# Kernel optimization log

Measured on AMD Instinct MI355X. Metric: run time of the kernel, lower is better.

The kernel has to match this reference:

```python
import jax, jax.numpy as jnp
import numpy as np

ALPHA = 0.0  # module init alpha
BETA = 1.0   # default beta in set_target_with_data


def setup_inputs() -> dict:
    key = jax.random.key(0)
    k1, k2, k3, k4 = jax.random.split(key, 4)
    B, H, KP, N, D = 4, 16, 512, 4096, 64
    return {
        "K": jax.random.normal(k1, (B, H, KP, D), dtype=jnp.float32),
        "V": jax.random.normal(k2, (B, H, KP, D), dtype=jnp.float32),
        "xk": jax.random.normal(k3, (B, H, N, D), dtype=jnp.float32),
        "xv": jax.random.normal(k4, (B, H, N, D), dtype=jnp.float32),
    }


def reference(K, V, xk, xv):
    # set_target_with_data with dist_metric='dot', beta=1.0, beta2=None
    # dists: (B, H, k, n) = K @ xk^T
    dists = jnp.einsum('bhkd,bhnd->bhkn', K, xk)
    # softmax over the memory-slot axis (dim=-2)
    dk = jax.nn.softmax(BETA * dists, axis=-2)
    # normalize over the data axis (dim=-1)
    dkx = dk / jnp.sum(dk, axis=-1, keepdims=True)
    # weighted readout of data queries/values
    K_target = jnp.einsum('bhkn,bhnd->bhkd', dkx, xk)
    V_target = jnp.einsum('bhkn,bhnd->bhkd', dkx, xv)
    # set_target: grads used by maximize-SGD update
    gK = (1.0 - ALPHA) * (K_target - K)
    gV = (1.0 - ALPHA) * (V_target - V)
    return jnp.stack((gK, gV), axis=0)  # (2, B, H, k, d)
```

## Files before the change

### kernel.cpp

```cpp
#include <hip/hip_runtime.h>
#include <hip/hip_bf16.h>

typedef __bf16 bf16_t;
typedef __attribute__((ext_vector_type(8))) __bf16 bf16x8;
typedef __attribute__((ext_vector_type(4))) float f32x4;
typedef __attribute__((ext_vector_type(16))) float f32x16;

#define BH 64
#define KP 512
#define NN 4096
#define DD 64
#define GSZ (BH * KP * DD)
#define NT 64

#define MFMA16(a, b, c) __builtin_amdgcn_mfma_f32_16x16x32_bf16((a), (b), (c), 0, 0, 0)
#define MFMA32(a, b, c) __builtin_amdgcn_mfma_f32_32x32x16_bf16((a), (b), (c), 0, 0, 0)

__device__ __forceinline__ bf16x8 cvt8v(const f32x4 lo, const f32x4 hi) {
  bf16x8 r;
  r[0] = (bf16_t)lo[0]; r[1] = (bf16_t)lo[1]; r[2] = (bf16_t)lo[2]; r[3] = (bf16_t)lo[3];
  r[4] = (bf16_t)hi[0]; r[5] = (bf16_t)hi[1]; r[6] = (bf16_t)hi[2]; r[7] = (bf16_t)hi[3];
  return r;
}
__device__ __forceinline__ bf16x8 cvt8(const float* __restrict__ p) {
  return cvt8v(*(const f32x4*)p, *(const f32x4*)(p + 4));
}
__device__ __forceinline__ unsigned pack2(float a, float b) {
  union { bf16_t h[2]; unsigned u; } x;
  x.h[0] = (bf16_t)a; x.h[1] = (bf16_t)b;
  return x.u;
}

__device__ __forceinline__ void stage16(bf16_t* lds_base, const bf16_t* gsrc) {
  __builtin_amdgcn_global_load_lds(
      (const __attribute__((address_space(1))) void*)gsrc,
      (__attribute__((address_space(3))) void*)lds_base, 16, 0, 0);
}

__global__ __launch_bounds__(256) void hop_p1f(
    const float* __restrict__ Km, const float* __restrict__ xk,
    const float* __restrict__ xv,
    bf16_t* __restrict__ xk16, bf16_t* __restrict__ xkT16,
    bf16_t* __restrict__ xvT16, float* __restrict__ inv_colsum)
{
  __shared__ __align__(16) bf16_t Ks[128 * 72];
  bf16_t* T = Ks;

  const int tid  = threadIdx.x;
  const int wave = tid >> 6, lane = tid & 63;
  const int col  = lane & 15, quad = lane >> 4;
  const int bid  = blockIdx.x;
  const int bh   = (bid & 7) + 8 * ((bid >> 3) & 7);
  const int nblk = (bid >> 6) * 256;

  const float* Kb  = Km + (size_t)bh * KP * DD;
  const size_t gb  = (size_t)bh * NN * DD;
  const size_t gbT = (size_t)bh * DD * NN;

  const int row  = tid >> 2;
  const int d0   = (tid & 3) * 16;
  const int dcol = tid >> 2;
  const int nb   = (tid & 3) * 16;

  bf16x8 bf[4][2];

  #pragma unroll
  for (int b = 0; b < 4; b++) {
    const int nbase = nblk + b * 64;
    {
      const float* src = xk + gb + (size_t)(nbase + row) * DD + d0;
      const f32x4 a0 = *(const f32x4*)(src);
      const f32x4 a1 = *(const f32x4*)(src + 4);
      const f32x4 a2 = *(const f32x4*)(src + 8);
      const f32x4 a3 = *(const f32x4*)(src + 12);
      const bf16x8 lo = cvt8v(a0, a1), hi = cvt8v(a2, a3);
      bf16_t* dn = xk16 + gb + (size_t)(nbase + row) * DD + d0;
      *(bf16x8*)(dn)     = lo;
      *(bf16x8*)(dn + 8) = hi;
      *(bf16x8*)(T + row * 72 + d0)     = lo;
      *(bf16x8*)(T + row * 72 + d0 + 8) = hi;
    }
    __syncthreads();
    {
      bf16x8 o0, o1;
      #pragma unroll
      for (int j = 0; j < 8; j++) o0[j] = T[(nb + j) * 72 + dcol];
      #pragma unroll
      for (int j = 0; j < 8; j++) o1[j] = T[(nb + 8 + j) * 72 + dcol];
      bf16_t* dT = xkT16 + gbT + (size_t)dcol * NN + nbase + nb;
      *(bf16x8*)(dT)     = o0;
      *(bf16x8*)(dT + 8) = o1;
      if (wave == b) {
        #pragma unroll
        for (int nsub = 0; nsub < 4; nsub++) {
          bf[nsub][0] = *(const bf16x8*)(T + (nsub * 16 + col) * 72 + quad * 8);
          bf[nsub][1] = *(const bf16x8*)(T + (nsub * 16 + col) * 72 + 32 + quad * 8);
        }
      }
    }
    __syncthreads();
    {
      const float* src = xv + gb + (size_t)(nbase + row) * DD + d0;
      const f32x4 a0 = *(const f32x4*)(src);
      const f32x4 a1 = *(const f32x4*)(src + 4);
      const f32x4 a2 = *(const f32x4*)(src + 8);
      const f32x4 a3 = *(const f32x4*)(src + 12);
      *(bf16x8*)(T + row * 72 + d0)     = cvt8v(a0, a1);
      *(bf16x8*)(T + row * 72 + d0 + 8) = cvt8v(a2, a3);
    }
    __syncthreads();
    {
      bf16x8 o0, o1;
      #pragma unroll
      for (int j = 0; j < 8; j++) o0[j] = T[(nb + j) * 72 + dcol];
      #pragma unroll
      for (int j = 0; j < 8; j++) o1[j] = T[(nb + 8 + j) * 72 + dcol];
      bf16_t* dT = xvT16 + gbT + (size_t)dcol * NN + nbase + nb;
      *(bf16x8*)(dT)     = o0;
      *(bf16x8*)(dT + 8) = o1;
    }
    __syncthreads();
  }

  float colacc[4] = {0.f, 0.f, 0.f, 0.f};
  const int srow = tid >> 1, sdo = (tid & 1) * 32;

  for (int kc = 0; kc < KP; kc += 128) {
    __syncthreads();
    const float* src = Kb + (size_t)(kc + srow) * DD + sdo;
    #pragma unroll
    for (int u = 0; u < 4; u++) {
      const f32x4 p0 = *(const f32x4*)(src + 8 * u);
      const f32x4 p1 = *(const f32x4*)(src + 8 * u + 4);
      *(bf16x8*)(Ks + srow * 72 + sdo + 8 * u) = cvt8v(p0, p1);
    }
    __syncthreads();
    #pragma unroll
    for (int ks = 0; ks < 8; ks++) {
      const bf16x8 a0 = *(const bf16x8*)(Ks + (ks * 16 + col) * 72 + quad * 8);
      const bf16x8 a1 = *(const bf16x8*)(Ks + (ks * 16 + col) * 72 + 32 + quad * 8);
      #pragma unroll
      for (int nsub = 0; nsub < 4; nsub++) {
        f32x4 c = {0.f, 0.f, 0.f, 0.f};
        c = MFMA16(a0, bf[nsub][0], c);
        c = MFMA16(a1, bf[nsub][1], c);
        colacc[nsub] += __expf(c[0]) + __expf(c[1]) + __expf(c[2]) + __expf(c[3]);
      }
    }
  }
  #pragma unroll
  for (int nsub = 0; nsub < 4; nsub++) {
    colacc[nsub] += __shfl_xor(colacc[nsub], 16, 64);
    colacc[nsub] += __shfl_xor(colacc[nsub], 32, 64);
  }
  float v = colacc[0];
  v = (quad == 1) ? colacc[1] : v;
  v = (quad == 2) ? colacc[2] : v;
  v = (quad == 3) ? colacc[3] : v;
  inv_colsum[bh * NN + nblk + wave * 64 + quad * 16 + col] = 1.0f / v;
}

template <int NS>
__global__ __launch_bounds__(256) void hop_pass2s(
    const float* __restrict__ Km,
    const bf16_t* __restrict__ xk16, const bf16_t* __restrict__ xkT16,
    const bf16_t* __restrict__ xvT16,
    const float* __restrict__ inv_colsum,
    float* __restrict__ pK, float* __restrict__ pV, float* __restrict__ prs)
{
  constexpr int NSEG = NN / NS;

  __shared__ __align__(16) bf16_t xks[2][NT * DD];
  __shared__ __align__(16) bf16_t xkT[2][DD * NT];
  __shared__ __align__(16) bf16_t xvT[2][DD * NT];

  const int tid  = threadIdx.x;
  const int wave = tid >> 6, lane = tid & 63;
  const int col  = lane & 31, hi = lane >> 5;
  const int bid  = blockIdx.x;
  const int bh   = (bid & 7) + 8 * ((bid >> 3) & 7);
  const int sub  = bid >> 6;
  const int kblk = sub & 3;
  const int nq   = sub >> 2;
  const int k0w  = kblk * 128 + wave * 32;
  const int nbase = nq * NSEG;

  const float*  Kb   = Km    + (size_t)bh * KP * DD;
  const bf16_t* xkb  = xk16  + (size_t)bh * NN * DD;
  const bf16_t* xkTb = xkT16 + (size_t)bh * DD * NN;
  const bf16_t* xvTb = xvT16 + (size_t)bh * DD * NN;
  const float*  inv  = inv_colsum + bh * NN;

  bf16x8 bk[4];
  #pragma unroll
  for (int t = 0; t < 4; t++)
    bk[t] = cvt8(Kb + (size_t)(k0w + col) * DD + t * 16 + hi * 8);

  f32x16 accK[2], accV[2];
  #pragma unroll
  for (int i = 0; i < 2; i++) {
    #pragma unroll
    for (int r = 0; r < 16; r++) { accK[i][r] = 0.f; accV[i][r] = 0.f; }
  }
  float rowacc = 0.f;

  const int srl = lane >> 3;
  const int r0  = wave * 16 + srl;
  const int r1  = r0 + 8;
  const int sb  = ((lane & 7) ^ srl) * 8;
  const int lb0 = (wave * 2 + 0) * 512;
  const int lb1 = (wave * 2 + 1) * 512;

  stage16(&xks[0][lb0], xkb + (size_t)(nbase + r0) * DD + sb);
  stage16(&xks[0][lb1], xkb + (size_t)(nbase + r1) * DD + sb);
  stage16(&xkT[0][lb0], xkTb + (size_t)r0 * NN + nbase + sb);
  stage16(&xkT[0][lb1], xkTb + (size_t)r1 * NN + nbase + sb);
  stage16(&xvT[0][lb0], xvTb + (size_t)r0 * NN + nbase + sb);
  stage16(&xvT[0][lb1], xvTb + (size_t)r1 * NN + nbase + sb);
  __syncthreads();

  int cur = 0;
  for (int n0 = nbase; n0 < nbase + NSEG; n0 += NT) {
    if (n0 + NT < nbase + NSEG) {
      const int nx = n0 + NT;
      const int nb2 = cur ^ 1;
      stage16(&xks[nb2][lb0], xkb + (size_t)(nx + r0) * DD + sb);
      stage16(&xks[nb2][lb1], xkb + (size_t)(nx + r1) * DD + sb);
      stage16(&xkT[nb2][lb0], xkTb + (size_t)r0 * NN + nx + sb);
      stage16(&xkT[nb2][lb1], xkTb + (size_t)r1 * NN + nx + sb);
      stage16(&xvT[nb2][lb0], xvTb + (size_t)r0 * NN + nx + sb);
      stage16(&xvT[nb2][lb1], xvTb + (size_t)r1 * NN + nx + sb);
    }

    const bf16_t* xs = xks[cur];
    bf16x8 wa[4];

    #pragma unroll
    for (int g = 0; g < 2; g++) {
      f32x4 icv[4];
      #pragma unroll
      for (int q = 0; q < 4; q++)
        icv[q] = *(const f32x4*)(inv + n0 + 32 * g + 8 * q + 4 * hi);

      const int n  = g * 32 + col;
      const int rb = n * DD;
      f32x16 s;
      #pragma unroll
      for (int r = 0; r < 16; r++) s[r] = 0.f;
      #pragma unroll
      for (int t = 0; t < 4; t++) {
        const bf16x8 a = *(const bf16x8*)(xs + rb + (((2 * t + hi) ^ (n & 7)) << 3));
        s = MFMA32(a, bk[t], s);
      }
      #pragma unroll
      for (int b = 0; b < 2; b++) {
        float p[8];
        #pragma unroll
        for (int j = 0; j < 8; j++)
          p[j] = __expf(s[8 * b + j]) * icv[2 * b + (j >> 2)][j & 3];
        rowacc += ((p[0] + p[1]) + (p[2] + p[3])) + ((p[4] + p[5]) + (p[6] + p[7]));
        unsigned q0a = pack2(p[0], p[1]), q0b = pack2(p[2], p[3]);
        unsigned q1a = pack2(p[4], p[5]), q1b = pack2(p[6], p[7]);
        asm("v_permlane32_swap_b32 %0, %1" : "+v"(q0a), "+v"(q1a));
        asm("v_permlane32_swap_b32 %0, %1" : "+v"(q0b), "+v"(q1b));
        union { unsigned u[4]; bf16x8 v; } f;
        f.u[0] = q0a; f.u[1] = q0b; f.u[2] = q1a; f.u[3] = q1b;
        wa[g * 2 + b] = f.v;
      }
    }

    #pragma unroll
    for (int dg = 0; dg < 2; dg++) {
      const int d   = dg * 32 + col;
      const int rbd = d * NT;
      const bf16_t* kp = xkT[cur];
      const bf16_t* vp = xvT[cur];
      #pragma unroll
      for (int c = 0; c < 4; c++) {
        const int off = rbd + (((2 * c + hi) ^ (d & 7)) << 3);
        const bf16x8 bkf = *(const bf16x8*)(kp + off);
        const bf16x8 bvf = *(const bf16x8*)(vp + off);
        accK[dg] = MFMA32(wa[c], bkf, accK[dg]);
        accV[dg] = MFMA32(wa[c], bvf, accV[dg]);
      }
    }

    __syncthreads();
    cur ^= 1;
  }

  rowacc += __shfl_xor(rowacc, 32, 64);
  if (hi == 0) prs[((size_t)nq * BH + bh) * KP + k0w + col] = rowacc;

  float* pKb = pK + ((size_t)(nq * BH + bh) * KP) * DD;
  float* pVb = pV + ((size_t)(nq * BH + bh) * KP) * DD;
  #pragma unroll
  for (int dg = 0; dg < 2; dg++) {
    #pragma unroll
    for (int r = 0; r < 16; r++) {
      const int kw = (r & 3) + 8 * (r >> 2) + 4 * hi;
      const int k = k0w + kw;
      const int d = dg * 32 + col;
      pKb[(size_t)k * DD + d] = accK[dg][r];
      pVb[(size_t)k * DD + d] = accV[dg][r];
    }
  }
}

template <int NS>
__global__ __launch_bounds__(256) void hop_fin(
    const float* __restrict__ Km, const float* __restrict__ Vm,
    const float* __restrict__ pK, const float* __restrict__ pV,
    const float* __restrict__ prs, float* __restrict__ out)
{
  const int t = blockIdx.x * 256 + threadIdx.x;
  const size_t e   = (size_t)t * 8;
  const size_t kk  = e >> 6;
  const size_t off = e;
  const size_t plane = (size_t)BH * KP * DD;

  float rs = 0.f;
  #pragma unroll
  for (int s = 0; s < NS; s++) rs += prs[(size_t)s * BH * KP + kk];
  const float invr = 1.0f / rs;

  f32x4 sk0 = {0.f, 0.f, 0.f, 0.f}, sk1 = {0.f, 0.f, 0.f, 0.f};
  f32x4 sv0 = {0.f, 0.f, 0.f, 0.f}, sv1 = {0.f, 0.f, 0.f, 0.f};
  #pragma unroll
  for (int s = 0; s < NS; s++) {
    sk0 += *(const f32x4*)(pK + (size_t)s * plane + off);
    sk1 += *(const f32x4*)(pK + (size_t)s * plane + off + 4);
    sv0 += *(const f32x4*)(pV + (size_t)s * plane + off);
    sv1 += *(const f32x4*)(pV + (size_t)s * plane + off + 4);
  }
  const f32x4 K0 = *(const f32x4*)(Km + off);
  const f32x4 K1 = *(const f32x4*)(Km + off + 4);
  const f32x4 V0 = *(const f32x4*)(Vm + off);
  const f32x4 V1 = *(const f32x4*)(Vm + off + 4);

  *(f32x4*)(out + off)           = sk0 * invr - K0;
  *(f32x4*)(out + off + 4)       = sk1 * invr - K1;
  *(f32x4*)(out + GSZ + off)     = sv0 * invr - V0;
  *(f32x4*)(out + GSZ + off + 4) = sv1 * invr - V1;
}

#define PW 72

__global__ __launch_bounds__(256) void hop_pass1_fb(
    const float* __restrict__ Km, const float* __restrict__ xk,
    float* __restrict__ inv_colsum)
{
  __shared__ __align__(16) bf16_t Ks[128 * 72];
  const int tid  = threadIdx.x;
  const int wave = tid >> 6, lane = tid & 63;
  const int col  = lane & 15, quad = lane >> 4;
  const int bh = blockIdx.y;
  const int n0 = blockIdx.x * 256 + wave * 64;
  const float* Kb  = Km + (size_t)bh * KP * DD;
  const float* xkb = xk + (size_t)bh * NN * DD;
  bf16x8 bf[4][2];
  #pragma unroll
  for (int nsub = 0; nsub < 4; nsub++) {
    const float* p = xkb + (size_t)(n0 + nsub * 16 + col) * DD + quad * 8;
    bf[nsub][0] = cvt8(p);
    bf[nsub][1] = cvt8(p + 32);
  }
  float colacc[4] = {0.f, 0.f, 0.f, 0.f};
  const int srow = tid >> 1, sdo = (tid & 1) * 32;
  for (int kc = 0; kc < KP; kc += 128) {
    __syncthreads();
    const float* src = Kb + (size_t)(kc + srow) * DD + sdo;
    #pragma unroll
    for (int u = 0; u < 4; u++) {
      const f32x4 p0 = *(const f32x4*)(src + 8 * u);
      const f32x4 p1 = *(const f32x4*)(src + 8 * u + 4);
      *(bf16x8*)(Ks + srow * 72 + sdo + 8 * u) = cvt8v(p0, p1);
    }
    __syncthreads();
    #pragma unroll
    for (int ks = 0; ks < 8; ks++) {
      const bf16x8 a0 = *(const bf16x8*)(Ks + (ks * 16 + col) * 72 + quad * 8);
      const bf16x8 a1 = *(const bf16x8*)(Ks + (ks * 16 + col) * 72 + 32 + quad * 8);
      #pragma unroll
      for (int nsub = 0; nsub < 4; nsub++) {
        f32x4 c = {0.f, 0.f, 0.f, 0.f};
        c = MFMA16(a0, bf[nsub][0], c);
        c = MFMA16(a1, bf[nsub][1], c);
        colacc[nsub] += __expf(c[0]) + __expf(c[1]) + __expf(c[2]) + __expf(c[3]);
      }
    }
  }
  #pragma unroll
  for (int nsub = 0; nsub < 4; nsub++) {
    colacc[nsub] += __shfl_xor(colacc[nsub], 16, 64);
    colacc[nsub] += __shfl_xor(colacc[nsub], 32, 64);
  }
  float v = colacc[0];
  v = (quad == 1) ? colacc[1] : v;
  v = (quad == 2) ? colacc[2] : v;
  v = (quad == 3) ? colacc[3] : v;
  inv_colsum[bh * NN + n0 + quad * 16 + col] = 1.0f / v;
}

__global__ __launch_bounds__(256) void hop_pass2_fb(
    const float* __restrict__ Km, const float* __restrict__ Vm,
    const float* __restrict__ xk, const float* __restrict__ xv,
    const float* __restrict__ inv_colsum, float* __restrict__ out)
{
  __shared__ __align__(16) bf16_t xksf[NT * PW];
  __shared__ __align__(16) bf16_t xkTf[DD * NT];
  __shared__ __align__(16) bf16_t xvTf[DD * NT];
  __shared__ __align__(16) bf16_t wtf[4][16 * PW];

  const int tid  = threadIdx.x;
  const int wave = tid >> 6, lane = tid & 63;
  const int col  = lane & 15, quad = lane >> 4;
  const int bh   = blockIdx.x >> 3;
  const int k0   = (blockIdx.x & 7) * 64 + wave * 16;

  const float* Kb  = Km + (size_t)bh * KP * DD;
  const float* Vb  = Vm + (size_t)bh * KP * DD;
  const float* xkb = xk + (size_t)bh * NN * DD;
  const float* xvb = xv + (size_t)bh * NN * DD;
  const float* inv = inv_colsum + bh * NN;

  const bf16x8 ak0 = cvt8(Kb + (size_t)(k0 + col) * DD + quad * 8);
  const bf16x8 ak1 = cvt8(Kb + (size_t)(k0 + col) * DD + 32 + quad * 8);

  f32x4 accK[4], accV[4];
  #pragma unroll
  for (int i = 0; i < 4; i++) {
    accK[i] = (f32x4){0.f, 0.f, 0.f, 0.f};
    accV[i] = (f32x4){0.f, 0.f, 0.f, 0.f};
  }
  float rows_part = 0.f;

  const int sn = tid >> 2;
  const int sd = (tid & 3) * 16;
  const int shi = sn >> 3, slo = sn & 7;

  for (int n0 = 0; n0 < NN; n0 += NT) {
    f32x4 gk[4], gv[4];
    #pragma unroll
    for (int u = 0; u < 4; u++) {
      gk[u] = *(const f32x4*)(xkb + (size_t)(n0 + sn) * DD + sd + 4 * u);
      gv[u] = *(const f32x4*)(xvb + (size_t)(n0 + sn) * DD + sd + 4 * u);
    }
    float ic[4];
    #pragma unroll
    for (int nsub = 0; nsub < 4; nsub++) ic[nsub] = inv[n0 + nsub * 16 + col];

    __syncthreads();
    *(bf16x8*)(xksf + sn * PW + sd)     = cvt8v(gk[0], gk[1]);
    *(bf16x8*)(xksf + sn * PW + sd + 8) = cvt8v(gk[2], gk[3]);
    #pragma unroll
    for (int j = 0; j < 16; j++) {
      const int d   = sd + j;
      const int off = d * NT + (((shi) ^ (d >> 3)) << 3) + slo;
      xkTf[off] = (bf16_t)gk[j >> 2][j & 3];
      xvTf[off] = (bf16_t)gv[j >> 2][j & 3];
    }
    __syncthreads();

    f32x4 s[4];
    #pragma unroll
    for (int nsub = 0; nsub < 4; nsub++) {
      const bf16x8 b0 = *(const bf16x8*)(xksf + (nsub * 16 + col) * PW + quad * 8);
      const bf16x8 b1 = *(const bf16x8*)(xksf + (nsub * 16 + col) * PW + 32 + quad * 8);
      f32x4 c = {0.f, 0.f, 0.f, 0.f};
      c = MFMA16(ak0, b0, c);
      c = MFMA16(ak1, b1, c);
      s[nsub] = c;
    }
    bf16_t* wr = wtf[wave];
    #pragma unroll
    for (int nsub = 0; nsub < 4; nsub++) {
      #pragma unroll
      for (int r = 0; r < 4; r++)
        wr[(quad * 4 + r) * PW + nsub * 16 + col] = (bf16_t)(__expf(s[nsub][r]) * ic[nsub]);
    }
    const bf16x8 wa0 = *(const bf16x8*)(wr + col * PW + quad * 8);
    const bf16x8 wa1 = *(const bf16x8*)(wr + col * PW + 32 + quad * 8);
    #pragma unroll
    for (int j = 0; j < 8; j++) rows_part += (float)wa0[j] + (float)wa1[j];

    #pragma unroll
    for (int dt = 0; dt < 4; dt++) {
      const int d = dt * 16 + col, dhi = d >> 3;
      const bf16x8 bk0 = *(const bf16x8*)(xkTf + d * NT + ((quad ^ dhi) << 3));
      const bf16x8 bk1 = *(const bf16x8*)(xkTf + d * NT + (((4 + quad) ^ dhi) << 3));
      const bf16x8 bv0 = *(const bf16x8*)(xvTf + d * NT + ((quad ^ dhi) << 3));
      const bf16x8 bv1 = *(const bf16x8*)(xvTf + d * NT + (((4 + quad) ^ dhi) << 3));
      accK[dt] = MFMA16(wa0, bk0, accK[dt]);
      accK[dt] = MFMA16(wa1, bk1, accK[dt]);
      accV[dt] = MFMA16(wa0, bv0, accV[dt]);
      accV[dt] = MFMA16(wa1, bv1, accV[dt]);
    }
  }

  float rs = rows_part;
  rs += __shfl_xor(rs, 16, 64);
  rs += __shfl_xor(rs, 32, 64);
  float invrs[4];
  #pragma unroll
  for (int r = 0; r < 4; r++) invrs[r] = 1.0f / __shfl(rs, quad * 4 + r, 64);

  const size_t base = (size_t)bh * KP * DD;
  #pragma unroll
  for (int dt = 0; dt < 4; dt++) {
    #pragma unroll
    for (int r = 0; r < 4; r++) {
      const int k = k0 + quad * 4 + r;
      const int d = dt * 16 + col;
      const size_t idx = base + (size_t)k * DD + d;
      out[idx]       = accK[dt][r] * invrs[r] - Kb[(size_t)k * DD + d];
      out[GSZ + idx] = accV[dt][r] * invrs[r] - Vb[(size_t)k * DD + d];
    }
  }
}

extern "C" void kernel_launch(void* const* d_in, const int* in_sizes, int n_in,
                              void* d_out, int out_size, void* d_ws, size_t ws_size,
                              hipStream_t stream)
{
  (void)in_sizes; (void)n_in; (void)out_size;
  const float* Km = (const float*)d_in[0];
  const float* Vm = (const float*)d_in[1];
  const float* xk = (const float*)d_in[2];
  const float* xv = (const float*)d_in[3];
  float* out = (float*)d_out;

  const size_t INVB  = (size_t)BH * NN * sizeof(float);
  const size_t SCRE  = (size_t)BH * NN * DD;
  const size_t BASE  = INVB + 3 * SCRE * sizeof(bf16_t);
  const size_t PLANE = (size_t)BH * KP * DD;
  const size_t NEED4 = BASE + (8 * PLANE + (size_t)4 * BH * KP) * sizeof(float);
  const size_t NEED2 = BASE + (4 * PLANE + (size_t)2 * BH * KP) * sizeof(float);

  float* inv_colsum = (float*)d_ws;

  if (ws_size >= NEED2) {
    bf16_t* xk16  = (bf16_t*)((char*)d_ws + INVB);
    bf16_t* xkT16 = xk16 + SCRE;
    bf16_t* xvT16 = xkT16 + SCRE;
    float*  pK    = (float*)(xvT16 + SCRE);

    hop_p1f<<<dim3(1024), 256, 0, stream>>>(Km, xk, xv, xk16, xkT16, xvT16,
                                            inv_colsum);
    if (ws_size >= NEED4) {
      float* pV  = pK + 4 * PLANE;
      float* prs = pV + 4 * PLANE;
      hop_pass2s<4><<<dim3(1024), 256, 0, stream>>>(Km, xk16, xkT16, xvT16,
                                                    inv_colsum, pK, pV, prs);
      hop_fin<4><<<dim3((BH * KP * DD) / (256 * 8)), 256, 0, stream>>>(
          Km, Vm, pK, pV, prs, out);
    } else {
      float* pV  = pK + 2 * PLANE;
      float* prs = pV + 2 * PLANE;
      hop_pass2s<2><<<dim3(512), 256, 0, stream>>>(Km, xk16, xkT16, xvT16,
                                                   inv_colsum, pK, pV, prs);
      hop_fin<2><<<dim3((BH * KP * DD) / (256 * 8)), 256, 0, stream>>>(
          Km, Vm, pK, pV, prs, out);
    }
  } else {
    hop_pass1_fb<<<dim3(NN / 256, BH), 256, 0, stream>>>(Km, xk, inv_colsum);
    hop_pass2_fb<<<dim3(BH * (KP / 64)), 256, 0, stream>>>(Km, Vm, xk, xv,
                                                           inv_colsum, out);
  }
}
```

Before: 317.3 us.

## Split prep from colsum pass and widen pass2 blocks to eight waves

The fused conversion plus column-sum kernel is split into a separate bf16 convert/transpose kernel and a column-sum kernel that reads the bf16 copy back from global memory. The second pass now uses 512-thread blocks covering 256 memory slots each, so every staged xk/xkT/xvT tile is shared by twice as many waves and fewer blocks are launched. This cuts redundant staging traffic and the serialized four-iteration prep loop in exchange for an extra launch, a global round trip of xk16, and possibly lower occupancy in pass2.

```diff
diff --git a/kernel.cpp b/kernel.cpp
--- a/kernel.cpp
+++ b/kernel.cpp
@@ -37,89 +37,90 @@
       (__attribute__((address_space(3))) void*)lds_base, 16, 0, 0);
 }
 
-__global__ __launch_bounds__(256) void hop_p1f(
-    const float* __restrict__ Km, const float* __restrict__ xk,
-    const float* __restrict__ xv,
-    bf16_t* __restrict__ xk16, bf16_t* __restrict__ xkT16,
-    bf16_t* __restrict__ xvT16, float* __restrict__ inv_colsum)
+__global__ __launch_bounds__(256) void hop_prep(
+    const float* __restrict__ xk, const float* __restrict__ xv,
+    bf16_t* __restrict__ xk16, bf16_t* __restrict__ xkT16, bf16_t* __restrict__ xvT16)
+{
+  __shared__ __align__(16) bf16_t T[64 * 72];
+  const int t = threadIdx.x;
+  const int n0 = blockIdx.x * 64;
+  const int bh = blockIdx.y;
+  const int row = t >> 2;
+  const int d0  = (t & 3) * 16;
+  const int dcol = t >> 2;
+  const int nb   = (t & 3) * 16;
+  const size_t gb  = (size_t)bh * NN * DD;
+  const size_t gbT = (size_t)bh * DD * NN;
+
+  {
+    const float* src = xk + gb + (size_t)(n0 + row) * DD + d0;
+    const f32x4 a0 = *(const f32x4*)(src);
+    const f32x4 a1 = *(const f32x4*)(src + 4);
+    const f32x4 a2 = *(const f32x4*)(src + 8);
+    const f32x4 a3 = *(const f32x4*)(src + 12);
+    const bf16x8 lo = cvt8v(a0, a1), hi = cvt8v(a2, a3);
+    bf16_t* dn = xk16 + gb + (size_t)(n0 + row) * DD + d0;
+    *(bf16x8*)(dn)     = lo;
+    *(bf16x8*)(dn + 8) = hi;
+    *(bf16x8*)(T + row * 72 + d0)     = lo;
+    *(bf16x8*)(T + row * 72 + d0 + 8) = hi;
+  }
+  __syncthreads();
+  {
+    bf16x8 o0, o1;
+    #pragma unroll
+    for (int j = 0; j < 8; j++) o0[j] = T[(nb + j) * 72 + dcol];
+    #pragma unroll
+    for (int j = 0; j < 8; j++) o1[j] = T[(nb + 8 + j) * 72 + dcol];
+    bf16_t* dT = xkT16 + gbT + (size_t)dcol * NN + n0 + nb;
+    *(bf16x8*)(dT)     = o0;
+    *(bf16x8*)(dT + 8) = o1;
+  }
+  __syncthreads();
+  {
+    const float* src = xv + gb + (size_t)(n0 + row) * DD + d0;
+    const f32x4 a0 = *(const f32x4*)(src);
+    const f32x4 a1 = *(const f32x4*)(src + 4);
+    const f32x4 a2 = *(const f32x4*)(src + 8);
+    const f32x4 a3 = *(const f32x4*)(src + 12);
+    *(bf16x8*)(T + row * 72 + d0)     = cvt8v(a0, a1);
+    *(bf16x8*)(T + row * 72 + d0 + 8) = cvt8v(a2, a3);
+  }
+  __syncthreads();
+  {
+    bf16x8 o0, o1;
+    #pragma unroll
+    for (int j = 0; j < 8; j++) o0[j] = T[(nb + j) * 72 + dcol];
+    #pragma unroll
+    for (int j = 0; j < 8; j++) o1[j] = T[(nb + 8 + j) * 72 + dcol];
+    bf16_t* dT = xvT16 + gbT + (size_t)dcol * NN + n0 + nb;
+    *(bf16x8*)(dT)     = o0;
+    *(bf16x8*)(dT + 8) = o1;
+  }
+}
+
+__global__ __launch_bounds__(256) void hop_pass1(
+    const float* __restrict__ Km, const bf16_t* __restrict__ xk16,
+    float* __restrict__ inv_colsum)
 {
   __shared__ __align__(16) bf16_t Ks[128 * 72];
-  bf16_t* T = Ks;
 
   const int tid  = threadIdx.x;
   const int wave = tid >> 6, lane = tid & 63;
   const int col  = lane & 15, quad = lane >> 4;
   const int bid  = blockIdx.x;
   const int bh   = (bid & 7) + 8 * ((bid >> 3) & 7);
-  const int nblk = (bid >> 6) * 256;
-
-  const float* Kb  = Km + (size_t)bh * KP * DD;
-  const size_t gb  = (size_t)bh * NN * DD;
-  const size_t gbT = (size_t)bh * DD * NN;
-
-  const int row  = tid >> 2;
-  const int d0   = (tid & 3) * 16;
-  const int dcol = tid >> 2;
-  const int nb   = (tid & 3) * 16;
+  const int n0   = (bid >> 6) * 256 + wave * 64;
+
+  const float*  Kb   = Km   + (size_t)bh * KP * DD;
+  const bf16_t* xkb  = xk16 + (size_t)bh * NN * DD;
 
   bf16x8 bf[4][2];
-
-  #pragma unroll
-  for (int b = 0; b < 4; b++) {
-    const int nbase = nblk + b * 64;
-    {
-      const float* src = xk + gb + (size_t)(nbase + row) * DD + d0;
-      const f32x4 a0 = *(const f32x4*)(src);
-      const f32x4 a1 = *(const f32x4*)(src + 4);
-      const f32x4 a2 = *(const f32x4*)(src + 8);
-      const f32x4 a3 = *(const f32x4*)(src + 12);
-      const bf16x8 lo = cvt8v(a0, a1), hi = cvt8v(a2, a3);
-      bf16_t* dn = xk16 + gb + (size_t)(nbase + row) * DD + d0;
-      *(bf16x8*)(dn)     = lo;
-      *(bf16x8*)(dn + 8) = hi;
-      *(bf16x8*)(T + row * 72 + d0)     = lo;
-      *(bf16x8*)(T + row * 72 + d0 + 8) = hi;
-    }
-    __syncthreads();
-    {
-      bf16x8 o0, o1;
-      #pragma unroll
-      for (int j = 0; j < 8; j++) o0[j] = T[(nb + j) * 72 + dcol];
-      #pragma unroll
-      for (int j = 0; j < 8; j++) o1[j] = T[(nb + 8 + j) * 72 + dcol];
-      bf16_t* dT = xkT16 + gbT + (size_t)dcol * NN + nbase + nb;
-      *(bf16x8*)(dT)     = o0;
-      *(bf16x8*)(dT + 8) = o1;
-      if (wave == b) {
-        #pragma unroll
-        for (int nsub = 0; nsub < 4; nsub++) {
-          bf[nsub][0] = *(const bf16x8*)(T + (nsub * 16 + col) * 72 + quad * 8);
-          bf[nsub][1] = *(const bf16x8*)(T + (nsub * 16 + col) * 72 + 32 + quad * 8);
-        }
-      }
-    }
-    __syncthreads();
-    {
-      const float* src = xv + gb + (size_t)(nbase + row) * DD + d0;
-      const f32x4 a0 = *(const f32x4*)(src);
-      const f32x4 a1 = *(const f32x4*)(src + 4);
-      const f32x4 a2 = *(const f32x4*)(src + 8);
-      const f32x4 a3 = *(const f32x4*)(src + 12);
-      *(bf16x8*)(T + row * 72 + d0)     = cvt8v(a0, a1);
-      *(bf16x8*)(T + row * 72 + d0 + 8) = cvt8v(a2, a3);
-    }
-    __syncthreads();
-    {
-      bf16x8 o0, o1;
-      #pragma unroll
-      for (int j = 0; j < 8; j++) o0[j] = T[(nb + j) * 72 + dcol];
-      #pragma unroll
-      for (int j = 0; j < 8; j++) o1[j] = T[(nb + 8 + j) * 72 + dcol];
-      bf16_t* dT = xvT16 + gbT + (size_t)dcol * NN + nbase + nb;
-      *(bf16x8*)(dT)     = o0;
-      *(bf16x8*)(dT + 8) = o1;
-    }
-    __syncthreads();
+  #pragma unroll
+  for (int nsub = 0; nsub < 4; nsub++) {
+    const bf16_t* p = xkb + (size_t)(n0 + nsub * 16 + col) * DD + quad * 8;
+    bf[nsub][0] = *(const bf16x8*)(p);
+    bf[nsub][1] = *(const bf16x8*)(p + 32);
   }
 
   float colacc[4] = {0.f, 0.f, 0.f, 0.f};
@@ -157,11 +158,11 @@
   v = (quad == 1) ? colacc[1] : v;
   v = (quad == 2) ? colacc[2] : v;
   v = (quad == 3) ? colacc[3] : v;
-  inv_colsum[bh * NN + nblk + wave * 64 + quad * 16 + col] = 1.0f / v;
+  inv_colsum[bh * NN + n0 + quad * 16 + col] = 1.0f / v;
 }
 
 template <int NS>
-__global__ __launch_bounds__(256) void hop_pass2s(
+__global__ __launch_bounds__(512) void hop_pass2w(
     const float* __restrict__ Km,
     const bf16_t* __restrict__ xk16, const bf16_t* __restrict__ xkT16,
     const bf16_t* __restrict__ xvT16,
@@ -180,9 +181,9 @@
   const int bid  = blockIdx.x;
   const int bh   = (bid & 7) + 8 * ((bid >> 3) & 7);
   const int sub  = bid >> 6;
-  const int kblk = sub & 3;
-  const int nq   = sub >> 2;
-  const int k0w  = kblk * 128 + wave * 32;
+  const int khalf = sub & 1;
+  const int nq    = sub >> 1;
+  const int k0w   = khalf * 256 + wave * 32;
   const int nbase = nq * NSEG;
 
   const float*  Kb   = Km    + (size_t)bh * KP * DD;
@@ -205,18 +206,13 @@
   float rowacc = 0.f;
 
   const int srl = lane >> 3;
-  const int r0  = wave * 16 + srl;
-  const int r1  = r0 + 8;
+  const int r0  = wave * 8 + srl;
   const int sb  = ((lane & 7) ^ srl) * 8;
-  const int lb0 = (wave * 2 + 0) * 512;
-  const int lb1 = (wave * 2 + 1) * 512;
-
-  stage16(&xks[0][lb0], xkb + (size_t)(nbase + r0) * DD + sb);
-  stage16(&xks[0][lb1], xkb + (size_t)(nbase + r1) * DD + sb);
-  stage16(&xkT[0][lb0], xkTb + (size_t)r0 * NN + nbase + sb);
-  stage16(&xkT[0][lb1], xkTb + (size_t)r1 * NN + nbase + sb);
-  stage16(&xvT[0][lb0], xvTb + (size_t)r0 * NN + nbase + sb);
-  stage16(&xvT[0][lb1], xvTb + (size_t)r1 * NN + nbase + sb);
+  const int lb  = wave * 512;
+
+  stage16(&xks[0][lb], xkb + (size_t)(nbase + r0) * DD + sb);
+  stage16(&xkT[0][lb], xkTb + (size_t)r0 * NN + nbase + sb);
+  stage16(&xvT[0][lb], xvTb + (size_t)r0 * NN + nbase + sb);
   __syncthreads();
 
   int cur = 0;
@@ -224,12 +220,9 @@
     if (n0 + NT < nbase + NSEG) {
       const int nx = n0 + NT;
       const int nb2 = cur ^ 1;
-      stage16(&xks[nb2][lb0], xkb + (size_t)(nx + r0) * DD + sb);
-      stage16(&xks[nb2][lb1], xkb + (size_t)(nx + r1) * DD + sb);
-      stage16(&xkT[nb2][lb0], xkTb + (size_t)r0 * NN + nx + sb);
-      stage16(&xkT[nb2][lb1], xkTb + (size_t)r1 * NN + nx + sb);
-      stage16(&xvT[nb2][lb0], xvTb + (size_t)r0 * NN + nx + sb);
-      stage16(&xvT[nb2][lb1], xvTb + (size_t)r1 * NN + nx + sb);
+      stage16(&xks[nb2][lb], xkb + (size_t)(nx + r0) * DD + sb);
+      stage16(&xkT[nb2][lb], xkTb + (size_t)r0 * NN + nx + sb);
+      stage16(&xvT[nb2][lb], xvTb + (size_t)r0 * NN + nx + sb);
     }
 
     const bf16_t* xs = xks[cur];
@@ -545,19 +538,19 @@
     bf16_t* xvT16 = xkT16 + SCRE;
     float*  pK    = (float*)(xvT16 + SCRE);
 
-    hop_p1f<<<dim3(1024), 256, 0, stream>>>(Km, xk, xv, xk16, xkT16, xvT16,
-                                            inv_colsum);
+    hop_prep<<<dim3(NN / 64, BH), 256, 0, stream>>>(xk, xv, xk16, xkT16, xvT16);
+    hop_pass1<<<dim3((NN / 256) * BH), 256, 0, stream>>>(Km, xk16, inv_colsum);
     if (ws_size >= NEED4) {
       float* pV  = pK + 4 * PLANE;
       float* prs = pV + 4 * PLANE;
-      hop_pass2s<4><<<dim3(1024), 256, 0, stream>>>(Km, xk16, xkT16, xvT16,
-                                                    inv_colsum, pK, pV, prs);
+      hop_pass2w<4><<<dim3(512), 512, 0, stream>>>(Km, xk16, xkT16, xvT16,
+                                                   inv_colsum, pK, pV, prs);
       hop_fin<4><<<dim3((BH * KP * DD) / (256 * 8)), 256, 0, stream>>>(
           Km, Vm, pK, pV, prs, out);
     } else {
       float* pV  = pK + 2 * PLANE;
       float* prs = pV + 2 * PLANE;
-      hop_pass2s<2><<<dim3(512), 256, 0, stream>>>(Km, xk16, xkT16, xvT16,
+      hop_pass2w<2><<<dim3(256), 512, 0, stream>>>(Km, xk16, xkT16, xvT16,
                                                    inv_colsum, pK, pV, prs);
       hop_fin<2><<<dim3((BH * KP * DD) / (256 * 8)), 256, 0, stream>>>(
           Km, Vm, pK, pV, prs, out);
```

Result: no change. 317.2 us (-0.0%).
